# Optimization experiments

Measured on AMD Instinct MI355X. Metric: run time of the kernel, lower is better.

Reference implementation:

```python
import jax, jax.numpy as jnp
import numpy as np

DIM = 4096
N_HEADS = 32
N_KV_HEADS = 8
HEAD_DIM = DIM // N_HEADS  # 128
B, S = 1, 2048
ROPE_THETA = 10000.0


def setup_inputs() -> dict:
    key = jax.random.key(0)
    kx, kq, kk, kv, ko = jax.random.split(key, 5)
    x = jax.random.normal(kx, (B, S, DIM), dtype=jnp.float32)
    # torch Linear weights are [out_features, in_features]
    wq = jax.random.normal(kq, (N_HEADS * HEAD_DIM, DIM), dtype=jnp.float32) * 0.02
    wk = jax.random.normal(kk, (N_KV_HEADS * HEAD_DIM, DIM), dtype=jnp.float32) * 0.02
    wv = jax.random.normal(kv, (N_KV_HEADS * HEAD_DIM, DIM), dtype=jnp.float32) * 0.02
    wo = jax.random.normal(ko, (DIM, N_HEADS * HEAD_DIM), dtype=jnp.float32) * 0.02
    # RoPE table [S, HEAD_DIM, 2]; frequencies repeated twice to match the
    # even/odd interleaved rotate_half convention of apply_rope.
    pos = jnp.arange(S, dtype=jnp.float32)
    inv_freq = 1.0 / (ROPE_THETA ** (jnp.arange(0, HEAD_DIM, 2, dtype=jnp.float32) / HEAD_DIM))
    ang = pos[:, None] * inv_freq[None, :]          # [S, HEAD_DIM/2]
    ang = jnp.repeat(ang, 2, axis=-1)               # [S, HEAD_DIM]
    rope_freqs = jnp.stack([jnp.cos(ang), jnp.sin(ang)], axis=-1)  # [S, HEAD_DIM, 2]
    return {"x": x, "wq": wq, "wk": wk, "wv": wv, "wo": wo,
            "rope_freqs": rope_freqs, "start_pos": 0}


def _rotate_half(t):
    # interleaved: (x0,x1,x2,x3,...) -> (-x1,x0,-x3,x2,...)
    t1 = t[..., ::2]
    t2 = t[..., 1::2]
    return jnp.stack((-t2, t1), axis=-1).reshape(t.shape)


def reference(x, wq, wk, wv, wo, rope_freqs, start_pos):
    b, s, _ = x.shape
    rep = N_HEADS // N_KV_HEADS
    scale = 1.0 / np.sqrt(HEAD_DIM)

    q = (x @ wq.T).reshape(b, s, N_HEADS, HEAD_DIM)
    k = (x @ wk.T).reshape(b, s, N_KV_HEADS, HEAD_DIM)
    v = (x @ wv.T).reshape(b, s, N_KV_HEADS, HEAD_DIM)

    cos = rope_freqs[..., 0][None, :, None, :]  # [1,S,1,HEAD_DIM]
    sin = rope_freqs[..., 1][None, :, None, :]
    q = q * cos + _rotate_half(q) * sin
    k = k * cos + _rotate_half(k) * sin

    # GQA without materializing repeated K/V: group query heads by kv head.
    qg = q.reshape(b, s, N_KV_HEADS, rep, HEAD_DIM)
    scores = jnp.einsum("bsgrd,btgd->bgrst", qg, k) * scale  # [B,KV,rep,S,S]
    causal = jnp.tril(jnp.ones((s, s), dtype=bool))
    scores = jnp.where(causal, scores, jnp.finfo(scores.dtype).min)
    attn = jax.nn.softmax(scores, axis=-1)
    out = jnp.einsum("bgrst,btgd->bsgrd", attn, v)           # [B,S,KV,rep,HEAD_DIM]
    out = out.reshape(b, s, N_HEADS * HEAD_DIM)
    return out @ wo.T
```

## Files before the change

### kernel.cpp

```cpp
#include <hip/hip_runtime.h>
#include <stdint.h>

#define DIM 4096
#define NH 32
#define NKV 8
#define HD 128
#define SEQ 2048
#define KVD 1024

typedef unsigned short u16;
typedef __attribute__((ext_vector_type(8))) short bf16x8;
typedef __attribute__((ext_vector_type(4))) float f32x4;

__device__ __forceinline__ float bf2f(u16 v){
  union { unsigned u; float f; } c; c.u = ((unsigned)v) << 16; return c.f;
}
__device__ __forceinline__ u16 f2bf(float f){
  union { float f; unsigned u; } c; c.f = f;
  unsigned u = c.u;
  u += 0x7FFF + ((u >> 16) & 1);
  return (u16)(u >> 16);
}
__device__ __forceinline__ unsigned pack2bf(float a, float b){
  return (unsigned)f2bf(a) | ((unsigned)f2bf(b) << 16);
}

__device__ __forceinline__ void gl_lds16(const void* g, void* l){
  __builtin_amdgcn_global_load_lds((const __attribute__((address_space(1))) void*)g,
                                   (__attribute__((address_space(3))) void*)l, 16, 0, 0);
}

#define VM0  asm volatile("s_waitcnt vmcnt(0)"  ::: "memory")
#define VM2  asm volatile("s_waitcnt vmcnt(2)"  ::: "memory")
#define VM7  asm volatile("s_waitcnt vmcnt(7)"  ::: "memory")
#define VM8  asm volatile("s_waitcnt vmcnt(8)"  ::: "memory")
#define VM10 asm volatile("s_waitcnt vmcnt(10)" ::: "memory")
#define VM12 asm volatile("s_waitcnt vmcnt(12)" ::: "memory")
#define LGKM0 asm volatile("s_waitcnt lgkmcnt(0)" ::: "memory")
#define SB0 __builtin_amdgcn_sched_barrier(0)
#define BAR __builtin_amdgcn_s_barrier()

__global__ void cvt_all(const float* __restrict__ x,  const float* __restrict__ wq,
                        const float* __restrict__ wk, const float* __restrict__ wv,
                        const float* __restrict__ wo,
                        u16* __restrict__ xb,  u16* __restrict__ wqb,
                        u16* __restrict__ wkb, u16* __restrict__ wvb,
                        u16* __restrict__ wob){
  const int b = blockIdx.x;
  const float* in; u16* out; int base;
  if      (b <  8192){ in = x;  out = xb;  base = b; }
  else if (b < 24576){ in = wq; out = wqb; base = b - 8192; }
  else if (b < 28672){ in = wk; out = wkb; base = b - 24576; }
  else if (b < 32768){ in = wv; out = wvb; base = b - 28672; }
  else               { in = wo; out = wob; base = b - 32768; }
  const int i = (base*256 + threadIdx.x)*4;
  float4 v = *(const float4*)(in + i);
  ushort4 o;
  o.x = f2bf(v.x); o.y = f2bf(v.y); o.z = f2bf(v.z); o.w = f2bf(v.w);
  *(ushort4*)(out + i) = o;
}

__global__ void add_f32(float* __restrict__ out, const float* __restrict__ p){
  const int i = blockIdx.x*256 + threadIdx.x;
  float4 a = ((const float4*)out)[i];
  const float4 b = ((const float4*)p)[i];
  a.x += b.x; a.y += b.y; a.z += b.z; a.w += b.w;
  ((float4*)out)[i] = a;
}

template<int BUNITS, int EPI>
__global__ __launch_bounds__(512, 2) void gemmP(const u16* __restrict__ A,
    const u16* __restrict__ B, void* __restrict__ C0, void* __restrict__ C1,
    void* __restrict__ C2, const float* __restrict__ rf, float* __restrict__ Cp){
  constexpr int BN = BUNITS*64;
  __shared__ __align__(16) char lds[65536 + BUNITS*16384];
  const int t = threadIdx.x, w = t >> 6, l = t & 63;
  const int lg = l >> 4, li = l & 15;
  const int wr = w >> 2, wc = w & 3;
  const int idx = ((int)blockIdx.x & 7)*32 + ((int)blockIdx.x >> 3);

  int bm, bn, kbase, nt, ks = 0;
  if (EPI == 0){ bm = idx & 7; bn = idx >> 3; kbase = 0; nt = 64; }
  else         { bm = idx & 7; ks = (idx >> 3) & 1; bn = idx >> 4; kbase = ks*2048; nt = 32; }
  const u16* Ab = A + (size_t)bm*256*DIM;
  const u16* Bb = B + (size_t)bn*BN*DIM;

  auto stA = [&](int k0, int abase, int u){
    const int r = u*64 + (t >> 3);
    gl_lds16(Ab + (size_t)r*DIM + k0 + (((t & 7) ^ (r & 7)) << 3),
             lds + abase + u*8192 + (t >> 3)*128 + (t & 7)*16);
  };
  auto stB = [&](int k0, int bbase, int u){
    const int r = u*64 + (t >> 3);
    gl_lds16(Bb + (size_t)r*DIM + k0 + (((t & 7) ^ (r & 7)) << 3),
             lds + bbase + u*8192 + (t >> 3)*128 + (t & 7)*16);
  };

  f32x4 acc[8][BUNITS] = {};
  bf16x8 bfr[BUNITS][2];

#define PH(p, ...) { \
    bf16x8 af[2][2]; \
    _Pragma("unroll") \
    for (int q = 0; q < 2; ++q){ \
      const int R = wr*128 + (2*(p)+q)*16 + li; \
      af[q][0] = *(const bf16x8*)(ldsA + R*128 + (( lg    ^ (R & 7)) << 4)); \
      af[q][1] = *(const bf16x8*)(ldsA + R*128 + (((lg+4) ^ (R & 7)) << 4)); \
    } \
    if ((p) == 0){ \
      _Pragma("unroll") \
      for (int j = 0; j < BUNITS; ++j){ \
        const int R = wc*(BUNITS*16) + j*16 + li; \
        bfr[j][0] = *(const bf16x8*)(ldsB + R*128 + (( lg    ^ (R & 7)) << 4)); \
        bfr[j][1] = *(const bf16x8*)(ldsB + R*128 + (((lg+4) ^ (R & 7)) << 4)); \
      } \
    } \
    __VA_ARGS__; \
    BAR; LGKM0; SB0; \
    __builtin_amdgcn_s_setprio(1); \
    _Pragma("unroll") \
    for (int q = 0; q < 2; ++q) \
      _Pragma("unroll") \
      for (int j = 0; j < BUNITS; ++j){ \
        acc[2*(p)+q][j] = __builtin_amdgcn_mfma_f32_16x16x32_bf16(af[q][0], bfr[j][0], acc[2*(p)+q][j], 0, 0, 0); \
        acc[2*(p)+q][j] = __builtin_amdgcn_mfma_f32_16x16x32_bf16(af[q][1], bfr[j][1], acc[2*(p)+q][j], 0, 0, 0); \
      } \
    __builtin_amdgcn_s_setprio(0); \
    BAR; }

  #pragma unroll
  for (int u = 0; u < BUNITS; ++u) stB(kbase, 65536, u);
  stA(kbase, 0, 0); stA(kbase, 0, 2);
  stA(kbase, 0, 1); stA(kbase, 0, 3);
  #pragma unroll
  for (int u = 0; u < BUNITS; ++u) stB(kbase + 64, 65536 + BUNITS*8192, u);
  stA(kbase + 64, 32768, 0); stA(kbase + 64, 32768, 2);
  if constexpr (BUNITS == 3) VM7; else VM8;
  BAR;

  for (int tt = 0; tt < nt; ++tt){
    const int k1 = kbase + (tt+1)*64, k2 = kbase + (tt+2)*64;
    const char* ldsA = lds + (tt & 1)*32768;
    const char* ldsB = lds + 65536 + (tt & 1)*BUNITS*8192;
    const int aCur = (tt & 1)*32768;
    const int aNxt = ((tt+1) & 1)*32768;
    const int bCur = 65536 + (tt & 1)*BUNITS*8192;

    PH(0, if (tt+1 < nt){ stA(k1, aNxt, 1); stA(k1, aNxt, 3); })
    PH(1, if (tt+2 < nt){ _Pragma("unroll")
                          for (int u = 0; u < BUNITS; ++u) stB(k2, bCur, u); }
          if (tt == nt-1){ VM0; }
          else if (tt == nt-2){ if constexpr (BUNITS == 3) VM7; else VM8; }
          else { if constexpr (BUNITS == 3) VM10; else VM12; } )
    PH(2, if (tt+2 < nt){ stA(k2, aCur, 0); stA(k2, aCur, 2); })
    PH(3, if (tt+1 < nt){
            if (tt+1 == nt-1){ VM2; }
            else { if constexpr (BUNITS == 3) VM7; else VM8; }
          } )
  }
#undef PH

  if (EPI == 1){
    float* C = (float*)(ks ? Cp : C0);
    #pragma unroll
    for (int i = 0; i < 8; ++i){
      const int srow = bm*256 + wr*128 + i*16 + lg*4;
      #pragma unroll
      for (int j = 0; j < BUNITS; ++j){
        const int col = bn*BN + wc*(BUNITS*16) + j*16 + li;
        #pragma unroll
        for (int r = 0; r < 4; ++r)
          C[(size_t)(srow + r)*DIM + col] = acc[i][j][r];
      }
    }
  } else {
    #pragma unroll
    for (int i = 0; i < 8; ++i){
      const int srow0 = bm*256 + wr*128 + i*16 + lg*4;
      #pragma unroll
      for (int j = 0; j < BUNITS; ++j){
        const int fc0 = bn*BN + wc*(BUNITS*16) + j*16;
        const int col = fc0 + li;
        if (fc0 < 5120){
          u16* C  = (fc0 < 4096) ? (u16*)C0 : (u16*)C1;
          const int ldc  = (fc0 < 4096) ? DIM : KVD;
          const int ccol = (fc0 < 4096) ? col : col - 4096;
          const int i4 = ((col & 127) >> 1) << 2;
          #pragma unroll
          for (int r = 0; r < 4; ++r){
            const float v = acc[i][j][r];
            const float p = __shfl_xor(v, 1);
            const int srow = srow0 + r;
            const float cs = rf[(size_t)srow*256 + i4];
            const float sn = rf[(size_t)srow*256 + i4 + 1];
            const float o = (col & 1) ? (v*cs + p*sn) : (v*cs - p*sn);
            C[(size_t)srow*ldc + ccol] = f2bf(o);
          }
        } else {
          u16* C = (u16*)C2;
          ushort4 o;
          o.x = f2bf(acc[i][j][0]); o.y = f2bf(acc[i][j][1]);
          o.z = f2bf(acc[i][j][2]); o.w = f2bf(acc[i][j][3]);
          *(ushort4*)&C[(size_t)(col - 5120)*SEQ + srow0] = o;
        }
      }
    }
  }
}

__global__ __launch_bounds__(256) void flash_attn(const u16* __restrict__ Q,
                                                  const u16* __restrict__ Kg,
                                                  const u16* __restrict__ Vt,
                                                  u16* __restrict__ O){
  __shared__ bf16x8 smK[2][64*16];
  __shared__ bf16x8 smV[2][128*8];
  __shared__ __align__(16) u16 smP[4][16*64];
  const int bid = blockIdx.x;
  const int h  = bid & 31;
  const int qt = 31 - (bid >> 5);
  const int g  = h >> 2;
  const int t = threadIdx.x, w = t >> 6, l = t & 63;
  const int lg = l >> 4, li = l & 15;

  bf16x8 qf[4];
  {
    const u16* qrow = Q + (size_t)(qt*64 + w*16 + li)*DIM + h*HD;
    #pragma unroll
    for (int kc = 0; kc < 4; ++kc)
      qf[kc] = *(const bf16x8*)(qrow + kc*32 + lg*8);
  }
  f32x4 accO[8] = {};
  float mrun = -1e30f, lsum = 0.f;
  const float SC = 0.08838834764831845f * 1.4426950408889634f;

  const int ksrow = t >> 4, ksslot = t & 15;
  const int vsrow = t >> 3, vsslot = t & 7;

  auto stage = [&](int kt, int b){
    #pragma unroll
    for (int j = 0; j < 4; ++j){
      const int krow = j*16 + ksrow;
      const int ksl = (ksslot & 8) | ((ksslot ^ (krow & 7)) & 7);
      gl_lds16(Kg + (size_t)(kt*64 + krow)*KVD + g*HD + ksl*8, (char*)&smK[b][0] + j*4096 + w*1024);
      const int vrow = j*32 + vsrow;
      const int vsl = (vsslot ^ (vrow & 7)) & 7;
      gl_lds16(Vt + (size_t)(g*HD + vrow)*SEQ + kt*64 + vsl*8, (char*)&smV[b][0] + j*4096 + w*1024);
    }
  };

  stage(0, 0);
  int buf = 0;
  u16* pw = &smP[w][0];

  for (int kt = 0; kt <= qt; ++kt){
    __syncthreads();
    if (kt < qt) stage(kt + 1, buf ^ 1);

    f32x4 sacc[4] = {};
    __builtin_amdgcn_s_setprio(1);
    #pragma unroll
    for (int kc = 0; kc < 4; ++kc){
      #pragma unroll
      for (int nj = 0; nj < 4; ++nj){
        const int R = nj*16 + li;
        int sl = lg + 4*kc;
        sl = (sl & 8) | ((sl ^ (R & 7)) & 7);
        sacc[nj] = __builtin_amdgcn_mfma_f32_16x16x32_bf16(smK[buf][R*16 + sl], qf[kc], sacc[nj], 0, 0, 0);
      }
    }
    __builtin_amdgcn_s_setprio(0);
    float p[4][4];
    #pragma unroll
    for (int nj = 0; nj < 4; ++nj)
      #pragma unroll
      for (int r = 0; r < 4; ++r)
        p[nj][r] = sacc[nj][r] * SC;
    if (kt == qt){
      const int qloc = w*16 + li;
      #pragma unroll
      for (int nj = 0; nj < 4; ++nj)
        #pragma unroll
        for (int r = 0; r < 4; ++r)
          if (nj*16 + lg*4 + r > qloc) p[nj][r] = -1e30f;
    }
    float mx = p[0][0];
    #pragma unroll
    for (int nj = 0; nj < 4; ++nj)
      #pragma unroll
      for (int r = 0; r < 4; ++r) mx = fmaxf(mx, p[nj][r]);
    mx = fmaxf(mx, __shfl_xor(mx, 16));
    mx = fmaxf(mx, __shfl_xor(mx, 32));
    if (!__all(mx - mrun <= 8.f)){
      const float mnew = fmaxf(mrun, mx);
      const float alpha = exp2f(mrun - mnew);
      lsum *= alpha;
      float al[4];
      #pragma unroll
      for (int r = 0; r < 4; ++r) al[r] = __shfl(alpha, (l & 48) | (lg*4 + r));
      #pragma unroll
      for (int dj = 0; dj < 8; ++dj)
        #pragma unroll
        for (int r = 0; r < 4; ++r) accO[dj][r] *= al[r];
      mrun = mnew;
    }
    float s = 0.f;
    #pragma unroll
    for (int nj = 0; nj < 4; ++nj)
      #pragma unroll
      for (int r = 0; r < 4; ++r){ p[nj][r] = exp2f(p[nj][r] - mrun); s += p[nj][r]; }
    s += __shfl_xor(s, 16);
    s += __shfl_xor(s, 32);
    lsum += s;
    #pragma unroll
    for (int nj = 0; nj < 4; ++nj){
      const int c = nj*2 + (lg >> 1);
      uint2 v; v.x = pack2bf(p[nj][0], p[nj][1]); v.y = pack2bf(p[nj][2], p[nj][3]);
      *(uint2*)((char*)pw + li*128 + ((c ^ (li & 7)) << 4) + ((lg & 1) << 3)) = v;
    }
    __builtin_amdgcn_s_setprio(1);
    #pragma unroll
    for (int kc2 = 0; kc2 < 2; ++kc2){
      const bf16x8 pf = *(const bf16x8*)((char*)pw + li*128 + (((kc2*4 + lg) ^ (li & 7)) << 4));
      #pragma unroll
      for (int dj = 0; dj < 8; ++dj){
        const int R = dj*16 + li;
        const bf16x8 vf = smV[buf][R*8 + ((lg + 4*kc2) ^ (R & 7))];
        accO[dj] = __builtin_amdgcn_mfma_f32_16x16x32_bf16(pf, vf, accO[dj], 0, 0, 0);
      }
    }
    __builtin_amdgcn_s_setprio(0);
    buf ^= 1;
  }
  float linv[4];
  #pragma unroll
  for (int r = 0; r < 4; ++r) linv[r] = 1.f / __shfl(lsum, (l & 48) | (lg*4 + r));
  #pragma unroll
  for (int dj = 0; dj < 8; ++dj)
    #pragma unroll
    for (int r = 0; r < 4; ++r)
      O[(size_t)(qt*64 + w*16 + lg*4 + r)*DIM + h*HD + dj*16 + li] = f2bf(accO[dj][r] * linv[r]);
}

extern "C" void kernel_launch(void* const* d_in, const int* in_sizes, int n_in,
                              void* d_out, int out_size, void* d_ws, size_t ws_size,
                              hipStream_t stream){
  const float* x  = (const float*)d_in[0];
  const float* wq = (const float*)d_in[1];
  const float* wk = (const float*)d_in[2];
  const float* wv = (const float*)d_in[3];
  const float* wo = (const float*)d_in[4];
  const float* rf = (const float*)d_in[5];
  float* out = (float*)d_out;

  char* ws = (char*)d_ws;
  size_t off = 0;
  auto alloc = [&](size_t nbytes){ void* p = ws + off; off += (nbytes + 255) & ~(size_t)255; return p; };
  u16* xb  = (u16*)alloc((size_t)SEQ*DIM*2);
  u16* wqb = (u16*)alloc((size_t)DIM*DIM*2);
  u16* wkb = (u16*)alloc((size_t)KVD*DIM*2);
  u16* wvb = (u16*)alloc((size_t)KVD*DIM*2);
  u16* wob = (u16*)alloc((size_t)DIM*DIM*2);
  u16* Qb  = (u16*)alloc((size_t)SEQ*DIM*2);
  u16* K8  = (u16*)alloc((size_t)SEQ*KVD*2);
  u16* Vtr = (u16*)alloc((size_t)KVD*SEQ*2);
  u16* AO  = (u16*)alloc((size_t)SEQ*DIM*2);
  float* P1 = (float*)wqb;

  cvt_all<<<49152, 256, 0, stream>>>(x, wq, wk, wv, wo, xb, wqb, wkb, wvb, wob);

  gemmP<3, 0><<<256, 512, 0, stream>>>(xb, wqb, Qb, K8, Vtr, rf, nullptr);

  flash_attn<<<SEQ/64 * NH, 256, 0, stream>>>(Qb, K8, Vtr, AO);

  gemmP<4, 1><<<256, 512, 0, stream>>>(AO, wob, out, nullptr, nullptr, nullptr, P1);
  add_f32<<<8192, 256, 0, stream>>>(out, P1);
}
```

Before: 305.7 us.

## Replace split-K output GEMM and add pass with full-K 128x256 tiled GEMM

The output projection previously used a 256x256 tile split into two K halves, writing one half to a scratch buffer and then summing with a separate add kernel. It now uses a dedicated kernel with 128x256 tiles over the full K range. This writes the fp32 result once and removes both the partial-sum round trip and the extra launch. Each block now runs twice as many K iterations, and with launch_bounds(512,1) and 96KB of LDS occupancy may be lower.

```diff
diff --git a/kernel.cpp b/kernel.cpp
--- a/kernel.cpp
+++ b/kernel.cpp
@@ -32,10 +32,9 @@
 
 #define VM0  asm volatile("s_waitcnt vmcnt(0)"  ::: "memory")
 #define VM2  asm volatile("s_waitcnt vmcnt(2)"  ::: "memory")
+#define VM4  asm volatile("s_waitcnt vmcnt(4)"  ::: "memory")
 #define VM7  asm volatile("s_waitcnt vmcnt(7)"  ::: "memory")
-#define VM8  asm volatile("s_waitcnt vmcnt(8)"  ::: "memory")
 #define VM10 asm volatile("s_waitcnt vmcnt(10)" ::: "memory")
-#define VM12 asm volatile("s_waitcnt vmcnt(12)" ::: "memory")
 #define LGKM0 asm volatile("s_waitcnt lgkmcnt(0)" ::: "memory")
 #define SB0 __builtin_amdgcn_sched_barrier(0)
 #define BAR __builtin_amdgcn_s_barrier()
@@ -60,28 +59,18 @@
   *(ushort4*)(out + i) = o;
 }
 
-__global__ void add_f32(float* __restrict__ out, const float* __restrict__ p){
-  const int i = blockIdx.x*256 + threadIdx.x;
-  float4 a = ((const float4*)out)[i];
-  const float4 b = ((const float4*)p)[i];
-  a.x += b.x; a.y += b.y; a.z += b.z; a.w += b.w;
-  ((float4*)out)[i] = a;
-}
-
-template<int BUNITS, int EPI>
+template<int BUNITS>
 __global__ __launch_bounds__(512, 2) void gemmP(const u16* __restrict__ A,
     const u16* __restrict__ B, void* __restrict__ C0, void* __restrict__ C1,
-    void* __restrict__ C2, const float* __restrict__ rf, float* __restrict__ Cp){
+    void* __restrict__ C2, const float* __restrict__ rf){
   constexpr int BN = BUNITS*64;
   __shared__ __align__(16) char lds[65536 + BUNITS*16384];
   const int t = threadIdx.x, w = t >> 6, l = t & 63;
   const int lg = l >> 4, li = l & 15;
   const int wr = w >> 2, wc = w & 3;
   const int idx = ((int)blockIdx.x & 7)*32 + ((int)blockIdx.x >> 3);
-
-  int bm, bn, kbase, nt, ks = 0;
-  if (EPI == 0){ bm = idx & 7; bn = idx >> 3; kbase = 0; nt = 64; }
-  else         { bm = idx & 7; ks = (idx >> 3) & 1; bn = idx >> 4; kbase = ks*2048; nt = 32; }
+  const int bm = idx & 7, bn = idx >> 3;
+  const int nt = 64, kbase = 0;
   const u16* Ab = A + (size_t)bm*256*DIM;
   const u16* Bb = B + (size_t)bn*BN*DIM;
 
@@ -135,7 +124,7 @@
   #pragma unroll
   for (int u = 0; u < BUNITS; ++u) stB(kbase + 64, 65536 + BUNITS*8192, u);
   stA(kbase + 64, 32768, 0); stA(kbase + 64, 32768, 2);
-  if constexpr (BUNITS == 3) VM7; else VM8;
+  VM7;
   BAR;
 
   for (int tt = 0; tt < nt; ++tt){
@@ -150,60 +139,135 @@
     PH(1, if (tt+2 < nt){ _Pragma("unroll")
                           for (int u = 0; u < BUNITS; ++u) stB(k2, bCur, u); }
           if (tt == nt-1){ VM0; }
-          else if (tt == nt-2){ if constexpr (BUNITS == 3) VM7; else VM8; }
-          else { if constexpr (BUNITS == 3) VM10; else VM12; } )
+          else if (tt == nt-2){ VM7; }
+          else { VM10; } )
     PH(2, if (tt+2 < nt){ stA(k2, aCur, 0); stA(k2, aCur, 2); })
     PH(3, if (tt+1 < nt){
             if (tt+1 == nt-1){ VM2; }
-            else { if constexpr (BUNITS == 3) VM7; else VM8; }
+            else { VM7; }
           } )
   }
 #undef PH
 
-  if (EPI == 1){
-    float* C = (float*)(ks ? Cp : C0);
-    #pragma unroll
-    for (int i = 0; i < 8; ++i){
-      const int srow = bm*256 + wr*128 + i*16 + lg*4;
-      #pragma unroll
-      for (int j = 0; j < BUNITS; ++j){
-        const int col = bn*BN + wc*(BUNITS*16) + j*16 + li;
+  #pragma unroll
+  for (int i = 0; i < 8; ++i){
+    const int srow0 = bm*256 + wr*128 + i*16 + lg*4;
+    #pragma unroll
+    for (int j = 0; j < BUNITS; ++j){
+      const int fc0 = bn*BN + wc*(BUNITS*16) + j*16;
+      const int col = fc0 + li;
+      if (fc0 < 5120){
+        u16* C  = (fc0 < 4096) ? (u16*)C0 : (u16*)C1;
+        const int ldc  = (fc0 < 4096) ? DIM : KVD;
+        const int ccol = (fc0 < 4096) ? col : col - 4096;
+        const int i4 = ((col & 127) >> 1) << 2;
         #pragma unroll
-        for (int r = 0; r < 4; ++r)
-          C[(size_t)(srow + r)*DIM + col] = acc[i][j][r];
+        for (int r = 0; r < 4; ++r){
+          const float v = acc[i][j][r];
+          const float p = __shfl_xor(v, 1);
+          const int srow = srow0 + r;
+          const float cs = rf[(size_t)srow*256 + i4];
+          const float sn = rf[(size_t)srow*256 + i4 + 1];
+          const float o = (col & 1) ? (v*cs + p*sn) : (v*cs - p*sn);
+          C[(size_t)srow*ldc + ccol] = f2bf(o);
+        }
+      } else {
+        u16* C = (u16*)C2;
+        ushort4 o;
+        o.x = f2bf(acc[i][j][0]); o.y = f2bf(acc[i][j][1]);
+        o.z = f2bf(acc[i][j][2]); o.w = f2bf(acc[i][j][3]);
+        *(ushort4*)&C[(size_t)(col - 5120)*SEQ + srow0] = o;
       }
     }
-  } else {
-    #pragma unroll
-    for (int i = 0; i < 8; ++i){
-      const int srow0 = bm*256 + wr*128 + i*16 + lg*4;
-      #pragma unroll
-      for (int j = 0; j < BUNITS; ++j){
-        const int fc0 = bn*BN + wc*(BUNITS*16) + j*16;
-        const int col = fc0 + li;
-        if (fc0 < 5120){
-          u16* C  = (fc0 < 4096) ? (u16*)C0 : (u16*)C1;
-          const int ldc  = (fc0 < 4096) ? DIM : KVD;
-          const int ccol = (fc0 < 4096) ? col : col - 4096;
-          const int i4 = ((col & 127) >> 1) << 2;
-          #pragma unroll
-          for (int r = 0; r < 4; ++r){
-            const float v = acc[i][j][r];
-            const float p = __shfl_xor(v, 1);
-            const int srow = srow0 + r;
-            const float cs = rf[(size_t)srow*256 + i4];
-            const float sn = rf[(size_t)srow*256 + i4 + 1];
-            const float o = (col & 1) ? (v*cs + p*sn) : (v*cs - p*sn);
-            C[(size_t)srow*ldc + ccol] = f2bf(o);
-          }
-        } else {
-          u16* C = (u16*)C2;
-          ushort4 o;
-          o.x = f2bf(acc[i][j][0]); o.y = f2bf(acc[i][j][1]);
-          o.z = f2bf(acc[i][j][2]); o.w = f2bf(acc[i][j][3]);
-          *(ushort4*)&C[(size_t)(col - 5120)*SEQ + srow0] = o;
-        }
-      }
+  }
+}
+
+__global__ __launch_bounds__(512, 1) void gemmO(const u16* __restrict__ A,
+    const u16* __restrict__ B, float* __restrict__ C){
+  __shared__ __align__(16) char lds[98304];
+  const int t = threadIdx.x, w = t >> 6, l = t & 63;
+  const int lg = l >> 4, li = l & 15;
+  const int wr = w >> 2, wc = w & 3;
+  const int idx = ((int)blockIdx.x & 7)*32 + ((int)blockIdx.x >> 3);
+  const int bm = idx & 15, bn = idx >> 4;
+  const int nt = 64;
+  const u16* Ab = A + (size_t)bm*128*DIM;
+  const u16* Bb = B + (size_t)bn*256*DIM;
+
+  auto stA2 = [&](int k0, int slot){
+    #pragma unroll
+    for (int j = 0; j < 2; ++j){
+      const int r = j*64 + (t >> 3);
+      gl_lds16(Ab + (size_t)r*DIM + k0 + (((t & 7) ^ (r & 7)) << 3),
+               lds + slot*16384 + r*128 + (t & 7)*16);
+    }
+  };
+  auto stB1 = [&](int k0, int slot, int u){
+    const int r = u*64 + (t >> 3);
+    gl_lds16(Bb + (size_t)r*DIM + k0 + (((t & 7) ^ (r & 7)) << 3),
+             lds + 32768 + slot*32768 + r*128 + (t & 7)*16);
+  };
+
+  f32x4 acc[4][4] = {};
+  bf16x8 bfr[4][2];
+
+#define PHO(p, ...) { \
+    bf16x8 af[2][2]; \
+    _Pragma("unroll") \
+    for (int q = 0; q < 2; ++q){ \
+      const int R = wr*64 + (2*(p)+q)*16 + li; \
+      af[q][0] = *(const bf16x8*)(ldsA + R*128 + (( lg    ^ (R & 7)) << 4)); \
+      af[q][1] = *(const bf16x8*)(ldsA + R*128 + (((lg+4) ^ (R & 7)) << 4)); \
+    } \
+    if ((p) == 0){ \
+      _Pragma("unroll") \
+      for (int j = 0; j < 4; ++j){ \
+        const int R = wc*64 + j*16 + li; \
+        bfr[j][0] = *(const bf16x8*)(ldsB + R*128 + (( lg    ^ (R & 7)) << 4)); \
+        bfr[j][1] = *(const bf16x8*)(ldsB + R*128 + (((lg+4) ^ (R & 7)) << 4)); \
+      } \
+    } \
+    __VA_ARGS__; \
+    BAR; LGKM0; SB0; \
+    __builtin_amdgcn_s_setprio(1); \
+    _Pragma("unroll") \
+    for (int q = 0; q < 2; ++q) \
+      _Pragma("unroll") \
+      for (int j = 0; j < 4; ++j){ \
+        acc[2*(p)+q][j] = __builtin_amdgcn_mfma_f32_16x16x32_bf16(af[q][0], bfr[j][0], acc[2*(p)+q][j], 0, 0, 0); \
+        acc[2*(p)+q][j] = __builtin_amdgcn_mfma_f32_16x16x32_bf16(af[q][1], bfr[j][1], acc[2*(p)+q][j], 0, 0, 0); \
+      } \
+    __builtin_amdgcn_s_setprio(0); \
+    BAR; }
+
+  #pragma unroll
+  for (int u = 0; u < 4; ++u) stB1(0, 0, u);
+  stA2(0, 0);
+  #pragma unroll
+  for (int u = 0; u < 4; ++u) stB1(64, 1, u);
+  VM4; BAR;
+
+  for (int tt = 0; tt < nt; ++tt){
+    const char* ldsA = lds + (tt & 1)*16384;
+    const char* ldsB = lds + 32768 + (tt & 1)*32768;
+    const int k1 = (tt+1)*64, k2 = (tt+2)*64;
+
+    PHO(0, if (tt+1 < nt){ stA2(k1, (tt+1) & 1); })
+    PHO(1, if (tt+2 < nt){ stB1(k2, tt & 1, 0); stB1(k2, tt & 1, 1);
+                           stB1(k2, tt & 1, 2); stB1(k2, tt & 1, 3); }
+           if (tt+1 < nt){ if (tt+2 < nt){ VM4; } else { VM0; } } )
+  }
+#undef PHO
+
+  #pragma unroll
+  for (int i = 0; i < 4; ++i){
+    const int srow = bm*128 + wr*64 + i*16 + lg*4;
+    #pragma unroll
+    for (int j = 0; j < 4; ++j){
+      const int col = bn*256 + wc*64 + j*16 + li;
+      #pragma unroll
+      for (int r = 0; r < 4; ++r)
+        C[(size_t)(srow + r)*DIM + col] = acc[i][j][r];
     }
   }
 }
@@ -364,14 +428,12 @@
   u16* K8  = (u16*)alloc((size_t)SEQ*KVD*2);
   u16* Vtr = (u16*)alloc((size_t)KVD*SEQ*2);
   u16* AO  = (u16*)alloc((size_t)SEQ*DIM*2);
-  float* P1 = (float*)wqb;
 
   cvt_all<<<49152, 256, 0, stream>>>(x, wq, wk, wv, wo, xb, wqb, wkb, wvb, wob);
 
-  gemmP<3, 0><<<256, 512, 0, stream>>>(xb, wqb, Qb, K8, Vtr, rf, nullptr);
+  gemmP<3><<<256, 512, 0, stream>>>(xb, wqb, Qb, K8, Vtr, rf);
 
   flash_attn<<<SEQ/64 * NH, 256, 0, stream>>>(Qb, K8, Vtr, AO);
 
-  gemmP<4, 1><<<256, 512, 0, stream>>>(AO, wob, out, nullptr, nullptr, nullptr, P1);
-  add_f32<<<8192, 256, 0, stream>>>(out, P1);
-}
+  gemmO<<<256, 512, 0, stream>>>(AO, wob, out);
+}
```

New measurement: 296.3 us, median of 2. 3.1% less time.
